# Kernel tuning notes

Hardware: AMD Instinct MI355X
Metric: run time of the kernel (lower is better)

The kernel has to match this reference:

```python
import jax, jax.numpy as jnp
import numpy as np

K = 3
ALPHA = 8.3

def _patches(x, oh, ow):
    # x: [B, C, H, W] -> [B, C, K, K, oh, ow] (stride=1, dilation=1)
    rows = []
    for k in range(K):
        cols = [x[:, :, k:k + oh, l:l + ow] for l in range(K)]
        rows.append(jnp.stack(cols, axis=2))  # [B, C, K, oh, ow]
    return jnp.stack(rows, axis=2)  # [B, C, K, K, oh, ow]

def setup_inputs() -> dict:
    key = jax.random.key(0)
    k1, k2, k3, k4 = jax.random.split(key, 4)
    B, C, H, W = 4, 64, 256, 256
    OC = 64
    img = jax.random.normal(k1, (B, C, H, W), dtype=jnp.float32)
    depth = jax.random.uniform(k2, (B, 1, H, W), dtype=jnp.float32)
    weight = jax.random.uniform(k3, (OC, C, K, K), dtype=jnp.float32, minval=-0.1, maxval=0.1)
    bias = jax.random.uniform(k4, (1, OC), dtype=jnp.float32, minval=-0.1, maxval=0.1)
    return {"img": img, "depth": depth, "weight": weight, "bias": bias}

def reference(img, depth, weight, bias):
    B, C, H, W = img.shape
    oh, ow = H - K + 1, W - K + 1
    c0 = K // 2
    img_p = _patches(img, oh, ow)                 # [B, C, K, K, oh, ow]
    dep_p = _patches(depth, oh, ow)[:, 0]         # [B, K, K, oh, ow]
    center = depth[:, 0, c0:c0 + oh, c0:c0 + ow]  # [B, oh, ow]
    dw = jnp.exp(-ALPHA * jnp.abs(dep_p - center[:, None, None]))  # [B, K, K, oh, ow]
    out = jnp.einsum('bcklpq,bklpq,ockl->bopq', img_p, dw, weight)
    out = out + bias[0][None, :, None, None]
    return out
```

## Files before the change

### kernel.cpp

```cpp
#include <hip/hip_runtime.h>
#include <hip/hip_bf16.h>

typedef __bf16 bf16_t;
typedef __bf16 bf16x4 __attribute__((ext_vector_type(4)));
typedef __bf16 bf16x8 __attribute__((ext_vector_type(8)));
typedef float f32x4 __attribute__((ext_vector_type(4)));

#define ALPHA 8.3f
#define CPAD 72
#define NCOL 136


__global__ void repack_w(const float* __restrict__ w, bf16_t* __restrict__ w2) {
    int idx = blockIdx.x * 256 + threadIdx.x;
    if (idx >= 9 * 2 * 4 * 64 * 8) return;
    int j     = idx & 7;
    int lane  = (idx >> 3) & 63;
    int m     = (idx >> 9) & 3;
    int chunk = (idx >> 11) & 1;
    int tap   = idx >> 12;
    int oc = m * 16 + (lane & 15);
    int c  = chunk * 32 + (lane >> 4) * 8 + j;
    int kt = tap / 3, lt = tap % 3;
    w2[idx] = (bf16_t)w[((oc * 64 + c) * 3 + kt) * 3 + lt];
}

__global__ __launch_bounds__(128) void depthconv_mfma(
    const float* __restrict__ img, const float* __restrict__ depth,
    const bf16_t* __restrict__ w2, const float* __restrict__ bias,
    float* __restrict__ out)
{
    __shared__ bf16_t lds[3 * NCOL * CPAD];

    const int tid = threadIdx.x;
    const int p = blockIdx.x >> 3;
    const int r = blockIdx.x & 7;
    const int b = r >> 1;
    const int h = r & 1;
    const int s0 = h ? 120 : 0;

    const float* imgb = img + (size_t)b * 64 * 65536;
    const float* dep  = depth + (size_t)b * 65536;

    for (int u = tid; u < 3 * 34 * 16; u += 128) {
        int cg   = u & 15;
        int colg = (u >> 4) % 34;
        int kt   = (u >> 4) / 34;
        int c0  = cg * 4;
        int cl0 = colg * 4;
        const float* src = imgb + (size_t)c0 * 65536 + (p + kt) * 256 + s0 + cl0;
        float4 v0 = *(const float4*)src;
        float4 v1 = *(const float4*)(src + 65536);
        float4 v2 = *(const float4*)(src + 2 * 65536);
        float4 v3 = *(const float4*)(src + 3 * 65536);
        bf16_t* dst = lds + (size_t)(kt * NCOL + cl0) * CPAD + c0;
        *(bf16x4*)(dst)            = (bf16x4){(bf16_t)v0.x, (bf16_t)v1.x, (bf16_t)v2.x, (bf16_t)v3.x};
        *(bf16x4*)(dst + CPAD)     = (bf16x4){(bf16_t)v0.y, (bf16_t)v1.y, (bf16_t)v2.y, (bf16_t)v3.y};
        *(bf16x4*)(dst + 2 * CPAD) = (bf16x4){(bf16_t)v0.z, (bf16_t)v1.z, (bf16_t)v2.z, (bf16_t)v3.z};
        *(bf16x4*)(dst + 3 * CPAD) = (bf16x4){(bf16_t)v0.w, (bf16_t)v1.w, (bf16_t)v2.w, (bf16_t)v3.w};
    }
    __syncthreads();

    const int wv   = tid >> 6;
    const int lane = tid & 63;
    const int n    = lane & 15;
    const int quad = lane >> 4;
    const int q0w  = h * 126 + wv * 64;
    const int clb0 = q0w - s0;

    float dc[4];
#pragma unroll
    for (int i = 0; i < 4; ++i)
        dc[i] = dep[(p + 1) * 256 + q0w + 16 * i + n + 1];

    f32x4 acc[4][4];
#pragma unroll
    for (int m = 0; m < 4; ++m)
#pragma unroll
        for (int i = 0; i < 4; ++i)
            acc[m][i] = (f32x4){0.f, 0.f, 0.f, 0.f};
    const f32x4 Z = (f32x4){0.f, 0.f, 0.f, 0.f};

    for (int kt = 0; kt < 3; ++kt) {
        float dwv[3][4];
#pragma unroll
        for (int lt = 0; lt < 3; ++lt)
#pragma unroll
            for (int i = 0; i < 4; ++i) {
                float d = dep[(p + kt) * 256 + q0w + 16 * i + n + lt];
                dwv[lt][i] = __expf(-ALPHA * fabsf(d - dc[i]));
            }
#pragma unroll
        for (int lt = 0; lt < 3; ++lt) {
            const int tap = kt * 3 + lt;
            f32x4 P[4][4];
#pragma unroll
            for (int chunk = 0; chunk < 2; ++chunk) {
                bf16x8 a[4];
                const bf16x8* w2p = (const bf16x8*)w2 + ((size_t)(tap * 2 + chunk) * 4) * 64 + lane;
#pragma unroll
                for (int m = 0; m < 4; ++m) a[m] = w2p[m * 64];
#pragma unroll
                for (int i = 0; i < 4; ++i) {
                    const bf16x8 bf = *(const bf16x8*)(
                        lds + (size_t)(kt * NCOL + clb0 + 16 * i + n + lt) * CPAD
                            + chunk * 32 + quad * 8);
                    if (chunk == 0) {
#pragma unroll
                        for (int m = 0; m < 4; ++m)
                            P[m][i] = __builtin_amdgcn_mfma_f32_16x16x32_bf16(a[m], bf, Z, 0, 0, 0);
                    } else {
#pragma unroll
                        for (int m = 0; m < 4; ++m)
                            P[m][i] = __builtin_amdgcn_mfma_f32_16x16x32_bf16(a[m], bf, P[m][i], 0, 0, 0);
                    }
                }
            }
#pragma unroll
            for (int m = 0; m < 4; ++m)
#pragma unroll
                for (int i = 0; i < 4; ++i)
                    acc[m][i] += dwv[lt][i] * P[m][i];
        }
    }

#pragma unroll
    for (int m = 0; m < 4; ++m) {
#pragma unroll
        for (int r2 = 0; r2 < 4; ++r2) {
            int oc = m * 16 + quad * 4 + r2;
            float bz = bias[oc];
#pragma unroll
            for (int i = 0; i < 4; ++i) {
                int q = q0w + 16 * i + n;
                out[((size_t)(b * 64 + oc) * 254 + p) * 254 + q] = acc[m][i][r2] + bz;
            }
        }
    }
}

extern "C" void kernel_launch(void* const* d_in, const int* in_sizes, int n_in,
                              void* d_out, int out_size, void* d_ws, size_t ws_size,
                              hipStream_t stream) {
    const float* img   = (const float*)d_in[0];
    const float* depth = (const float*)d_in[1];
    const float* w     = (const float*)d_in[2];
    const float* bias  = (const float*)d_in[3];
    bf16_t* w2 = (bf16_t*)d_ws;

    repack_w<<<144, 256, 0, stream>>>(w, w2);
    depthconv_mfma<<<2032, 128, 0, stream>>>(img, depth, w2, bias, (float*)d_out);
}
```

Before: 176.9 us.

## Stream 8-row output strips per block with rolling LDS row buffer and prefetch

Each block now covers an 8-row strip of output rows and keeps a 6-slot rolling LDS buffer of bf16-converted input rows. Each new row is loaded and converted once and reused across the three kernel rows, instead of every block reloading three input rows. Global loads for the next two rows are issued into registers before the current rows' MFMA work and written to LDS after it, overlapping load latency with compute. The grid shrinks to 256 blocks of 256 threads with launch_bounds(256,1), which lowers occupancy and adds register pressure from the 80-register staging buffer.

```diff
diff --git a/kernel.cpp b/kernel.cpp
--- a/kernel.cpp
+++ b/kernel.cpp
@@ -9,6 +9,7 @@
 #define ALPHA 8.3f
 #define CPAD 72
 #define NCOL 136
+#define NROW 6
 
 
 __global__ void repack_w(const float* __restrict__ w, bf16_t* __restrict__ w2) {
@@ -25,117 +26,164 @@
     w2[idx] = (bf16_t)w[((oc * 64 + c) * 3 + kt) * 3 + lt];
 }
 
-__global__ __launch_bounds__(128) void depthconv_mfma(
+__device__ __forceinline__ void stage_issue(const float* __restrict__ imgb, int r0,
+                                            int rmax, int s0, int tid, f32x4 sv[5][4]) {
+#pragma unroll
+    for (int k = 0; k < 5; ++k) {
+        int u = tid + (k << 8);
+        int ru = u >= 544;
+        int v = u - (ru ? 544 : 0);
+        int cg = v & 15, colg = v >> 4;
+        int row = r0 + ru;
+        if (u < 1088 && row <= rmax) {
+            const float* src = imgb + (size_t)(cg * 4) * 65536 + row * 256 + s0 + colg * 4;
+            sv[k][0] = *(const f32x4*)src;
+            sv[k][1] = *(const f32x4*)(src + 65536);
+            sv[k][2] = *(const f32x4*)(src + 2 * 65536);
+            sv[k][3] = *(const f32x4*)(src + 3 * 65536);
+        }
+    }
+}
+
+__device__ __forceinline__ void stage_commit(bf16_t* __restrict__ lds, int r0,
+                                             int rmax, int tid, const f32x4 sv[5][4]) {
+#pragma unroll
+    for (int k = 0; k < 5; ++k) {
+        int u = tid + (k << 8);
+        int ru = u >= 544;
+        int v = u - (ru ? 544 : 0);
+        int cg = v & 15, colg = v >> 4;
+        int row = r0 + ru;
+        if (u < 1088 && row <= rmax) {
+            int slot = row % NROW;
+            bf16_t* dst = lds + (size_t)(slot * NCOL + colg * 4) * CPAD + cg * 4;
+#pragma unroll
+            for (int i = 0; i < 4; ++i)
+                *(bf16x4*)(dst + i * CPAD) =
+                    (bf16x4){(bf16_t)sv[k][0][i], (bf16_t)sv[k][1][i],
+                             (bf16_t)sv[k][2][i], (bf16_t)sv[k][3][i]};
+        }
+    }
+}
+
+__global__ __launch_bounds__(256, 1) void depthconv_mfma(
     const float* __restrict__ img, const float* __restrict__ depth,
     const bf16_t* __restrict__ w2, const float* __restrict__ bias,
     float* __restrict__ out)
 {
-    __shared__ bf16_t lds[3 * NCOL * CPAD];
+    __shared__ bf16_t lds[NROW * NCOL * CPAD];
 
     const int tid = threadIdx.x;
-    const int p = blockIdx.x >> 3;
-    const int r = blockIdx.x & 7;
-    const int b = r >> 1;
-    const int h = r & 1;
-    const int s0 = h ? 120 : 0;
+    const int blk   = blockIdx.x;
+    const int strip = blk >> 3;
+    const int b     = (blk >> 1) & 3;
+    const int h     = blk & 1;
+    const int p0    = strip * 8;
+    const int pend  = min(p0 + 7, 253);
+    const int rmax  = pend + 2;
+    const int s0    = h ? 120 : 0;
 
     const float* imgb = img + (size_t)b * 64 * 65536;
     const float* dep  = depth + (size_t)b * 65536;
 
-    for (int u = tid; u < 3 * 34 * 16; u += 128) {
-        int cg   = u & 15;
-        int colg = (u >> 4) % 34;
-        int kt   = (u >> 4) / 34;
-        int c0  = cg * 4;
-        int cl0 = colg * 4;
-        const float* src = imgb + (size_t)c0 * 65536 + (p + kt) * 256 + s0 + cl0;
-        float4 v0 = *(const float4*)src;
-        float4 v1 = *(const float4*)(src + 65536);
-        float4 v2 = *(const float4*)(src + 2 * 65536);
-        float4 v3 = *(const float4*)(src + 3 * 65536);
-        bf16_t* dst = lds + (size_t)(kt * NCOL + cl0) * CPAD + c0;
-        *(bf16x4*)(dst)            = (bf16x4){(bf16_t)v0.x, (bf16_t)v1.x, (bf16_t)v2.x, (bf16_t)v3.x};
-        *(bf16x4*)(dst + CPAD)     = (bf16x4){(bf16_t)v0.y, (bf16_t)v1.y, (bf16_t)v2.y, (bf16_t)v3.y};
-        *(bf16x4*)(dst + 2 * CPAD) = (bf16x4){(bf16_t)v0.z, (bf16_t)v1.z, (bf16_t)v2.z, (bf16_t)v3.z};
-        *(bf16x4*)(dst + 3 * CPAD) = (bf16x4){(bf16_t)v0.w, (bf16_t)v1.w, (bf16_t)v2.w, (bf16_t)v3.w};
-    }
+    f32x4 sv[5][4];
+    stage_issue(imgb, p0, rmax, s0, tid, sv);
+    stage_commit(lds, p0, rmax, tid, sv);
+    stage_issue(imgb, p0 + 2, rmax, s0, tid, sv);
+    stage_commit(lds, p0 + 2, rmax, tid, sv);
     __syncthreads();
 
     const int wv   = tid >> 6;
     const int lane = tid & 63;
+    const int pr   = wv >> 1;
+    const int qt   = wv & 1;
     const int n    = lane & 15;
     const int quad = lane >> 4;
-    const int q0w  = h * 126 + wv * 64;
+    const int q0w  = h * 126 + qt * 64;
     const int clb0 = q0w - s0;
 
-    float dc[4];
-#pragma unroll
-    for (int i = 0; i < 4; ++i)
-        dc[i] = dep[(p + 1) * 256 + q0w + 16 * i + n + 1];
-
-    f32x4 acc[4][4];
-#pragma unroll
-    for (int m = 0; m < 4; ++m)
+    const f32x4 Z = (f32x4){0.f, 0.f, 0.f, 0.f};
+
+    for (int p = p0; p <= pend; p += 2) {
+        const int r0 = p + 4;
+        const bool st = (r0 <= rmax);
+        if (st) stage_issue(imgb, r0, rmax, s0, tid, sv);
+
+        const int prow = p + pr;
+        float dc[4];
 #pragma unroll
         for (int i = 0; i < 4; ++i)
-            acc[m][i] = (f32x4){0.f, 0.f, 0.f, 0.f};
-    const f32x4 Z = (f32x4){0.f, 0.f, 0.f, 0.f};
-
-    for (int kt = 0; kt < 3; ++kt) {
-        float dwv[3][4];
-#pragma unroll
-        for (int lt = 0; lt < 3; ++lt)
-#pragma unroll
-            for (int i = 0; i < 4; ++i) {
-                float d = dep[(p + kt) * 256 + q0w + 16 * i + n + lt];
-                dwv[lt][i] = __expf(-ALPHA * fabsf(d - dc[i]));
-            }
-#pragma unroll
-        for (int lt = 0; lt < 3; ++lt) {
-            const int tap = kt * 3 + lt;
-            f32x4 P[4][4];
-#pragma unroll
-            for (int chunk = 0; chunk < 2; ++chunk) {
-                bf16x8 a[4];
-                const bf16x8* w2p = (const bf16x8*)w2 + ((size_t)(tap * 2 + chunk) * 4) * 64 + lane;
-#pragma unroll
-                for (int m = 0; m < 4; ++m) a[m] = w2p[m * 64];
+            dc[i] = dep[(prow + 1) * 256 + q0w + 16 * i + n + 1];
+
+        f32x4 acc[4][4];
+#pragma unroll
+        for (int m = 0; m < 4; ++m)
+#pragma unroll
+            for (int i = 0; i < 4; ++i) acc[m][i] = Z;
+
+        for (int kt = 0; kt < 3; ++kt) {
+            const int rs = (prow + kt) % NROW;
+            float dwv[3][4];
+#pragma unroll
+            for (int lt = 0; lt < 3; ++lt)
 #pragma unroll
                 for (int i = 0; i < 4; ++i) {
-                    const bf16x8 bf = *(const bf16x8*)(
-                        lds + (size_t)(kt * NCOL + clb0 + 16 * i + n + lt) * CPAD
-                            + chunk * 32 + quad * 8);
-                    if (chunk == 0) {
-#pragma unroll
-                        for (int m = 0; m < 4; ++m)
-                            P[m][i] = __builtin_amdgcn_mfma_f32_16x16x32_bf16(a[m], bf, Z, 0, 0, 0);
-                    } else {
-#pragma unroll
-                        for (int m = 0; m < 4; ++m)
-                            P[m][i] = __builtin_amdgcn_mfma_f32_16x16x32_bf16(a[m], bf, P[m][i], 0, 0, 0);
+                    float d = dep[(prow + kt) * 256 + q0w + 16 * i + n + lt];
+                    dwv[lt][i] = __expf(-ALPHA * fabsf(d - dc[i]));
+                }
+#pragma unroll
+            for (int lt = 0; lt < 3; ++lt) {
+                const int tap = kt * 3 + lt;
+                f32x4 P[4][4];
+#pragma unroll
+                for (int chunk = 0; chunk < 2; ++chunk) {
+                    bf16x8 a[4];
+                    const bf16x8* w2p =
+                        (const bf16x8*)w2 + ((size_t)(tap * 2 + chunk) * 4) * 64 + lane;
+#pragma unroll
+                    for (int m = 0; m < 4; ++m) a[m] = w2p[m * 64];
+#pragma unroll
+                    for (int i = 0; i < 4; ++i) {
+                        const bf16x8 bf = *(const bf16x8*)(
+                            lds + (size_t)(rs * NCOL + clb0 + 16 * i + n + lt) * CPAD
+                                + chunk * 32 + quad * 8);
+                        if (chunk == 0) {
+#pragma unroll
+                            for (int m = 0; m < 4; ++m)
+                                P[m][i] = __builtin_amdgcn_mfma_f32_16x16x32_bf16(
+                                    a[m], bf, Z, 0, 0, 0);
+                        } else {
+#pragma unroll
+                            for (int m = 0; m < 4; ++m)
+                                P[m][i] = __builtin_amdgcn_mfma_f32_16x16x32_bf16(
+                                    a[m], bf, P[m][i], 0, 0, 0);
+                        }
                     }
                 }
+#pragma unroll
+                for (int m = 0; m < 4; ++m)
+#pragma unroll
+                    for (int i = 0; i < 4; ++i)
+                        acc[m][i] += dwv[lt][i] * P[m][i];
             }
-#pragma unroll
-            for (int m = 0; m < 4; ++m)
-#pragma unroll
-                for (int i = 0; i < 4; ++i)
-                    acc[m][i] += dwv[lt][i] * P[m][i];
-        }
-    }
-
-#pragma unroll
-    for (int m = 0; m < 4; ++m) {
-#pragma unroll
-        for (int r2 = 0; r2 < 4; ++r2) {
-            int oc = m * 16 + quad * 4 + r2;
-            float bz = bias[oc];
-#pragma unroll
-            for (int i = 0; i < 4; ++i) {
-                int q = q0w + 16 * i + n;
-                out[((size_t)(b * 64 + oc) * 254 + p) * 254 + q] = acc[m][i][r2] + bz;
+        }
+
+#pragma unroll
+        for (int m = 0; m < 4; ++m) {
+#pragma unroll
+            for (int r2 = 0; r2 < 4; ++r2) {
+                int oc = m * 16 + quad * 4 + r2;
+                float bz = bias[oc];
+#pragma unroll
+                for (int i = 0; i < 4; ++i) {
+                    int q = q0w + 16 * i + n;
+                    out[((size_t)(b * 64 + oc) * 254 + prow) * 254 + q] = acc[m][i][r2] + bz;
+                }
             }
         }
+
+        if (st) stage_commit(lds, r0, rmax, tid, sv);
+        __syncthreads();
     }
 }
 
@@ -149,5 +197,5 @@
     bf16_t* w2 = (bf16_t*)d_ws;
 
     repack_w<<<144, 256, 0, stream>>>(w, w2);
-    depthconv_mfma<<<2032, 128, 0, stream>>>(img, depth, w2, bias, (float*)d_out);
-}
+    depthconv_mfma<<<256, 256, 0, stream>>>(img, depth, w2, bias, (float*)d_out);
+}
```

After: 167.2 us. 5.5% less time.

## Retile conv blocks to two output rows by 64 columns with four waves

Applied to the files above, without the earlier changes.

Each block now covers two output rows and a 64-column strip, with 256 threads. Four input rows are staged in LDS and shared across both rows, instead of three rows per single output row. Each wave handles one output row and half of the output channels, which halves the accumulator registers so that launch_bounds can request 4 blocks per CU. This cuts redundant image loads (4 rows for 2 outputs instead of 3 for 1) and aims at higher occupancy. In exchange, each wave reloads the weight fragments, and the last column tile overlaps the previous one, so some columns are computed twice.

```diff
diff --git a/kernel.cpp b/kernel.cpp
--- a/kernel.cpp
+++ b/kernel.cpp
@@ -8,7 +8,7 @@
 
 #define ALPHA 8.3f
 #define CPAD 72
-#define NCOL 136
+#define NCOL 68
 
 
 __global__ void repack_w(const float* __restrict__ w, bf16_t* __restrict__ w2) {
@@ -25,61 +25,68 @@
     w2[idx] = (bf16_t)w[((oc * 64 + c) * 3 + kt) * 3 + lt];
 }
 
-__global__ __launch_bounds__(128) void depthconv_mfma(
+__global__ __launch_bounds__(256, 4) void depthconv_mfma(
     const float* __restrict__ img, const float* __restrict__ depth,
     const bf16_t* __restrict__ w2, const float* __restrict__ bias,
     float* __restrict__ out)
 {
-    __shared__ bf16_t lds[3 * NCOL * CPAD];
+    __shared__ bf16_t lds[4 * NCOL * CPAD];
 
     const int tid = threadIdx.x;
-    const int p = blockIdx.x >> 3;
-    const int r = blockIdx.x & 7;
-    const int b = r >> 1;
-    const int h = r & 1;
-    const int s0 = h ? 120 : 0;
+    const int blk   = blockIdx.x;
+    const int ppair = blk >> 4;
+    const int r     = blk & 15;
+    const int b     = r >> 2;
+    const int qt    = r & 3;
+    const int p0    = ppair * 2;
+    const int q0    = (qt == 3) ? 190 : qt * 64;
+    const int s0    = (qt == 3) ? 188 : q0;
 
     const float* imgb = img + (size_t)b * 64 * 65536;
     const float* dep  = depth + (size_t)b * 65536;
 
-    for (int u = tid; u < 3 * 34 * 16; u += 128) {
-        int cg   = u & 15;
-        int colg = (u >> 4) % 34;
-        int kt   = (u >> 4) / 34;
-        int c0  = cg * 4;
-        int cl0 = colg * 4;
-        const float* src = imgb + (size_t)c0 * 65536 + (p + kt) * 256 + s0 + cl0;
-        float4 v0 = *(const float4*)src;
-        float4 v1 = *(const float4*)(src + 65536);
-        float4 v2 = *(const float4*)(src + 2 * 65536);
-        float4 v3 = *(const float4*)(src + 3 * 65536);
-        bf16_t* dst = lds + (size_t)(kt * NCOL + cl0) * CPAD + c0;
-        *(bf16x4*)(dst)            = (bf16x4){(bf16_t)v0.x, (bf16_t)v1.x, (bf16_t)v2.x, (bf16_t)v3.x};
-        *(bf16x4*)(dst + CPAD)     = (bf16x4){(bf16_t)v0.y, (bf16_t)v1.y, (bf16_t)v2.y, (bf16_t)v3.y};
-        *(bf16x4*)(dst + 2 * CPAD) = (bf16x4){(bf16_t)v0.z, (bf16_t)v1.z, (bf16_t)v2.z, (bf16_t)v3.z};
-        *(bf16x4*)(dst + 3 * CPAD) = (bf16x4){(bf16_t)v0.w, (bf16_t)v1.w, (bf16_t)v2.w, (bf16_t)v3.w};
+#pragma unroll
+    for (int k = 0; k < 5; ++k) {
+        int u = tid + (k << 8);
+        if (u < 1088) {
+            int cg   = u & 15;
+            int rest = u >> 4;
+            int colg = rest % 17;
+            int row  = rest / 17;
+            const float* src = imgb + (size_t)(cg * 4) * 65536 + (p0 + row) * 256 + s0 + colg * 4;
+            f32x4 v0 = *(const f32x4*)src;
+            f32x4 v1 = *(const f32x4*)(src + 65536);
+            f32x4 v2 = *(const f32x4*)(src + 2 * 65536);
+            f32x4 v3 = *(const f32x4*)(src + 3 * 65536);
+            bf16_t* dst = lds + (size_t)(row * NCOL + colg * 4) * CPAD + cg * 4;
+#pragma unroll
+            for (int i = 0; i < 4; ++i)
+                *(bf16x4*)(dst + i * CPAD) =
+                    (bf16x4){(bf16_t)v0[i], (bf16_t)v1[i], (bf16_t)v2[i], (bf16_t)v3[i]};
+        }
     }
     __syncthreads();
 
     const int wv   = tid >> 6;
     const int lane = tid & 63;
+    const int pr   = wv >> 1;
+    const int mh   = wv & 1;
     const int n    = lane & 15;
     const int quad = lane >> 4;
-    const int q0w  = h * 126 + wv * 64;
-    const int clb0 = q0w - s0;
+    const int prow = p0 + pr;
+    const int clb0 = q0 - s0;
 
     float dc[4];
 #pragma unroll
     for (int i = 0; i < 4; ++i)
-        dc[i] = dep[(p + 1) * 256 + q0w + 16 * i + n + 1];
+        dc[i] = dep[(prow + 1) * 256 + q0 + 16 * i + n + 1];
 
-    f32x4 acc[4][4];
+    const f32x4 Z = (f32x4){0.f, 0.f, 0.f, 0.f};
+    f32x4 acc[2][4];
 #pragma unroll
-    for (int m = 0; m < 4; ++m)
+    for (int mm = 0; mm < 2; ++mm)
 #pragma unroll
-        for (int i = 0; i < 4; ++i)
-            acc[m][i] = (f32x4){0.f, 0.f, 0.f, 0.f};
-    const f32x4 Z = (f32x4){0.f, 0.f, 0.f, 0.f};
+        for (int i = 0; i < 4; ++i) acc[mm][i] = Z;
 
     for (int kt = 0; kt < 3; ++kt) {
         float dwv[3][4];
@@ -87,53 +94,51 @@
         for (int lt = 0; lt < 3; ++lt)
 #pragma unroll
             for (int i = 0; i < 4; ++i) {
-                float d = dep[(p + kt) * 256 + q0w + 16 * i + n + lt];
+                float d = dep[(prow + kt) * 256 + q0 + 16 * i + n + lt];
                 dwv[lt][i] = __expf(-ALPHA * fabsf(d - dc[i]));
             }
 #pragma unroll
         for (int lt = 0; lt < 3; ++lt) {
             const int tap = kt * 3 + lt;
-            f32x4 P[4][4];
+            f32x4 P[2][4];
 #pragma unroll
             for (int chunk = 0; chunk < 2; ++chunk) {
-                bf16x8 a[4];
-                const bf16x8* w2p = (const bf16x8*)w2 + ((size_t)(tap * 2 + chunk) * 4) * 64 + lane;
-#pragma unroll
-                for (int m = 0; m < 4; ++m) a[m] = w2p[m * 64];
+                const bf16x8* w2p = (const bf16x8*)w2
+                    + ((size_t)((tap * 2 + chunk) * 4 + mh * 2)) * 64 + lane;
+                bf16x8 a0 = w2p[0];
+                bf16x8 a1 = w2p[64];
 #pragma unroll
                 for (int i = 0; i < 4; ++i) {
                     const bf16x8 bf = *(const bf16x8*)(
-                        lds + (size_t)(kt * NCOL + clb0 + 16 * i + n + lt) * CPAD
+                        lds + (size_t)((pr + kt) * NCOL + clb0 + 16 * i + n + lt) * CPAD
                             + chunk * 32 + quad * 8);
                     if (chunk == 0) {
-#pragma unroll
-                        for (int m = 0; m < 4; ++m)
-                            P[m][i] = __builtin_amdgcn_mfma_f32_16x16x32_bf16(a[m], bf, Z, 0, 0, 0);
+                        P[0][i] = __builtin_amdgcn_mfma_f32_16x16x32_bf16(a0, bf, Z, 0, 0, 0);
+                        P[1][i] = __builtin_amdgcn_mfma_f32_16x16x32_bf16(a1, bf, Z, 0, 0, 0);
                     } else {
-#pragma unroll
-                        for (int m = 0; m < 4; ++m)
-                            P[m][i] = __builtin_amdgcn_mfma_f32_16x16x32_bf16(a[m], bf, P[m][i], 0, 0, 0);
+                        P[0][i] = __builtin_amdgcn_mfma_f32_16x16x32_bf16(a0, bf, P[0][i], 0, 0, 0);
+                        P[1][i] = __builtin_amdgcn_mfma_f32_16x16x32_bf16(a1, bf, P[1][i], 0, 0, 0);
                     }
                 }
             }
 #pragma unroll
-            for (int m = 0; m < 4; ++m)
+            for (int mm = 0; mm < 2; ++mm)
 #pragma unroll
                 for (int i = 0; i < 4; ++i)
-                    acc[m][i] += dwv[lt][i] * P[m][i];
+                    acc[mm][i] += dwv[lt][i] * P[mm][i];
         }
     }
 
 #pragma unroll
-    for (int m = 0; m < 4; ++m) {
+    for (int mm = 0; mm < 2; ++mm) {
 #pragma unroll
         for (int r2 = 0; r2 < 4; ++r2) {
-            int oc = m * 16 + quad * 4 + r2;
+            int oc = (mh * 2 + mm) * 16 + quad * 4 + r2;
             float bz = bias[oc];
 #pragma unroll
             for (int i = 0; i < 4; ++i) {
-                int q = q0w + 16 * i + n;
-                out[((size_t)(b * 64 + oc) * 254 + p) * 254 + q] = acc[m][i][r2] + bz;
+                int q = q0 + 16 * i + n;
+                out[((size_t)(b * 64 + oc) * 254 + prow) * 254 + q] = acc[mm][i][r2] + bz;
             }
         }
     }
@@ -149,5 +154,5 @@
     bf16_t* w2 = (bf16_t*)d_ws;
 
     repack_w<<<144, 256, 0, stream>>>(w, w2);
-    depthconv_mfma<<<2032, 128, 0, stream>>>(img, depth, w2, bias, (float*)d_out);
+    depthconv_mfma<<<2032, 256, 0, stream>>>(img, depth, w2, bias, (float*)d_out);
 }
```

Result: slower. 360.5 us (+103.7%).
